# Performance work log

Hardware: AMD Instinct MI355X
Metric: run time of the kernel (lower is better)

## Reference

```python
import jax, jax.numpy as jnp
import numpy as np

PT_SEQ_LEN = 16    # hardcoded hw_seq_len in the module
THETA = 10000.0


def _rope_tables(head_dim):
    # VisionRotaryEmbeddingFast with dim = head_dim // 2, pt_seq_len = ft_seq_len = 16
    d = head_dim // 2                                   # 32
    freqs = 1.0 / (THETA ** (np.arange(0, d, 2, dtype=np.float64) / d))  # (d//2,) = (16,)
    t = np.arange(PT_SEQ_LEN, dtype=np.float64)         # t / ft * pt = arange since ft==pt
    f = np.einsum('i,j->ij', t, freqs)                  # (16, 16)
    f = np.repeat(f, 2, axis=-1)                        # (16, 32)  '... n -> ... (n r)'
    fa = np.broadcast_to(f[:, None, :], (PT_SEQ_LEN, PT_SEQ_LEN, d))
    fb = np.broadcast_to(f[None, :, :], (PT_SEQ_LEN, PT_SEQ_LEN, d))
    full = np.concatenate([fa, fb], axis=-1).reshape(-1, head_dim)  # (256, head_dim)
    return (jnp.asarray(np.cos(full), dtype=jnp.float32),
            jnp.asarray(np.sin(full), dtype=jnp.float32))


def _rotate_half(x):
    # '... (d r) -> ... d r', r=2; (x1, x2) -> (-x2, x1)
    x = x.reshape(*x.shape[:-1], -1, 2)
    x1, x2 = x[..., 0], x[..., 1]
    return jnp.stack((-x2, x1), axis=-1).reshape(*x.shape[:-2], -1)


def _apply_rope(t, cos, sin):
    # t: (B, H, N, hd); cos/sin: (N, hd)
    return t * cos + _rotate_half(t) * sin


def setup_inputs() -> dict:
    key = jax.random.key(0)
    ks = jax.random.split(key, 5)
    B, N, dim, sem = 64, 256, 1024, 768
    return {
        'q': jax.random.normal(ks[0], (B, N, dim), dtype=jnp.float32),
        'kv': jax.random.normal(ks[1], (B, N, sem), dtype=jnp.float32),
        'Wq': jax.random.normal(ks[2], (dim, dim), dtype=jnp.float32) * 0.02,
        'Wkv': jax.random.normal(ks[3], (sem, 2 * dim), dtype=jnp.float32) * 0.02,
        'Wproj': jax.random.normal(ks[4], (dim, dim), dtype=jnp.float32) * 0.02,
        'bproj': jnp.zeros((dim,), dtype=jnp.float32),
    }


def reference(q, kv, Wq, Wkv, Wproj, bproj):
    B, N, C = q.shape
    H = 16
    hd = C // H
    cos, sin = _rope_tables(hd)

    qh = (q @ Wq).reshape(B, N, H, hd).transpose(0, 2, 1, 3)        # (B,H,N,hd)
    kvh = (kv @ Wkv).reshape(B, N, 2, H, hd).transpose(2, 0, 3, 1, 4)
    k, v = kvh[0], kvh[1]                                           # (B,H,N,hd)

    qh = _apply_rope(qh, cos, sin)
    k = _apply_rope(k, cos, sin)

    scale = 1.0 / jnp.sqrt(jnp.float32(hd))  # F.sdpa default scale
    logits = jnp.einsum('bhqd,bhkd->bhqk', qh, k) * scale
    attn = jax.nn.softmax(logits, axis=-1)
    out = jnp.einsum('bhqk,bhkd->bhqd', attn, v)                    # (B,H,N,hd)
    out = out.transpose(0, 2, 1, 3).reshape(B, N, C)
    return out @ Wproj + bproj
```

## Files before the change

### kernel.cpp

```cpp
#include <hip/hip_runtime.h>
#include <hip/hip_bf16.h>
#include <math.h>


typedef unsigned int uint;
typedef __attribute__((ext_vector_type(4)))  short s16x4;
typedef __attribute__((ext_vector_type(8)))  short s16x8;
typedef __attribute__((ext_vector_type(16))) short s16x16;
typedef __attribute__((ext_vector_type(4)))  float f32x4;

#define AS1 __attribute__((address_space(1)))
#define AS3 __attribute__((address_space(3)))

__device__ __forceinline__ short f2bf(float x){
  union{float f;uint u;}v; v.f=x;
  return (short)((v.u + 0x7FFFu + ((v.u>>16)&1u))>>16);
}
__device__ __forceinline__ float bf2f(short s){
  union{float f;uint u;}v; v.u=((uint)(unsigned short)s)<<16; return v.f;
}
__device__ __forceinline__ uint packbf(float a,float b){
  return (uint)(unsigned short)f2bf(a) | ((uint)(unsigned short)f2bf(b)<<16);
}
__device__ __forceinline__ void gl_lds16(const void* g, void* l){
  __builtin_amdgcn_global_load_lds((const AS1 uint*)g, (AS3 uint*)l, 16, 0, 0);
}
__device__ __forceinline__ s16x8 ld16(const short* p){ return *(const s16x8*)p; }

__global__ void k_detect(const uint* q, int* flag){
  __shared__ int cnt;
  if(threadIdx.x==0) cnt=0;
  __syncthreads();
  int c=0;
  for(int i=threadIdx.x;i<4096;i+=256){
    uint e=(q[i]>>7)&0xFFu;
    if(e>=120u && e<=130u) c++;
  }
  atomicAdd(&cnt,c);
  __syncthreads();
  if(threadIdx.x==0) *flag = (cnt>2048)?0:1;
}

__global__ void k_convert(const void* src, short* dst, long n8, const int* flag){
  int f=*flag;
  long stride=(long)gridDim.x*blockDim.x;
  for(long i=(long)blockIdx.x*blockDim.x+threadIdx.x;i<n8;i+=stride){
    s16x8 o;
    if(f){
      const float4* s=(const float4*)src;
      float4 a=s[i*2], b=s[i*2+1];
      o[0]=f2bf(a.x);o[1]=f2bf(a.y);o[2]=f2bf(a.z);o[3]=f2bf(a.w);
      o[4]=f2bf(b.x);o[5]=f2bf(b.y);o[6]=f2bf(b.z);o[7]=f2bf(b.w);
    }else{
      o=((const s16x8*)src)[i];
    }
    ((s16x8*)dst)[i]=o;
  }
}

__global__ void k_transpose(const void* W, short* WT, int K, int Nn, const int* flag){
  int f=*flag;
  long total=(long)Nn*(K/8);
  long stride=(long)gridDim.x*blockDim.x;
  for(long idx=(long)blockIdx.x*blockDim.x+threadIdx.x;idx<total;idx+=stride){
    int n=(int)(idx%Nn); int kc=(int)(idx/Nn); int k0=kc*8;
    s16x8 o;
    #pragma unroll
    for(int j=0;j<8;j++){
      o[j]= f ? f2bf(((const float*)W)[(long)(k0+j)*Nn+n])
              : ((const short*)W)[(long)(k0+j)*Nn+n];
    }
    *(s16x8*)&WT[(long)n*K+k0]=o;
  }
}

__global__ void k_tables(float* cosT, float* sinT){
  int t=blockIdx.x*blockDim.x+threadIdx.x;
  if(t>=256*64) return;
  int n=t>>6, d=t&63;
  int i=n>>4, j=n&15;
  int p=(d&31)>>1;
  double fr=pow(10000.0, -(double)(2*p)/32.0);
  double tt=(d<32)?(double)i:(double)j;
  double a=tt*fr;
  cosT[t]=(float)cos(a);
  sinT[t]=(float)sin(a);
}

__global__ void k_bias(const void* b, float* bo, const int* flag){
  int t=blockIdx.x*blockDim.x+threadIdx.x;
  if(t<1024) bo[t] = (*flag)? ((const float*)b)[t] : bf2f(((const short*)b)[t]);
}

#define BAR   __builtin_amdgcn_s_barrier()
#define LGKM0 asm volatile("s_waitcnt lgkmcnt(0)" ::: "memory")
#define VMC4  asm volatile("s_waitcnt vmcnt(4)" ::: "memory")
#define PRIO1 __builtin_amdgcn_s_setprio(1)
#define PRIO0 __builtin_amdgcn_s_setprio(0)

#define MM(H,V,BR) do{ \
  _Pragma("unroll") for(int ks_=0;ks_<2;ks_++){ \
    _Pragma("unroll") for(int mf_=0;mf_<4;mf_++){ \
      _Pragma("unroll") for(int nf_=0;nf_<2;nf_++){ \
        acc[(H)*4+mf_][(V)*2+nf_]=__builtin_amdgcn_mfma_f32_16x16x32_bf16( \
          aR[mf_][ks_],BR[nf_][ks_],acc[(H)*4+mf_][(V)*2+nf_],0,0,0); \
  }}} }while(0)

#define HALFIT(BUF,TA,TB) do{ \
  const short* RA=&lds[BUF][0][wm][0]; \
  const short* RB=&lds[BUF][1][0][0]; \
  ldA(RA,0,aR); ldB(RB,0,bR0); stage(0,0,TA); \
  BAR; LGKM0; PRIO1; MM(0,0,bR0); PRIO0; BAR; \
  ldB(RB,1,bR1); stage(0,1,TA); \
  BAR; LGKM0; PRIO1; MM(0,1,bR1); PRIO0; BAR; \
  ldA(RA,1,aR); stage(1,0,TB); \
  BAR; LGKM0; PRIO1; MM(1,1,bR1); PRIO0; BAR; \
  stage(1,1,TB); \
  BAR; PRIO1; MM(1,0,bR0); PRIO0; VMC4; BAR; \
}while(0)

template<int EPI>
__launch_bounds__(512,2)
__global__ void k_gemm8(const short* __restrict__ A, const short* __restrict__ BT,
                        const int Kdim, const int lgN,
                        short* __restrict__ out0, short* __restrict__ out1,
                        const float* __restrict__ cosT, const float* __restrict__ sinT,
                        const float* __restrict__ bias, const int* __restrict__ flag,
                        void* __restrict__ dout){
  __shared__ __align__(16) short lds[2][2][2][8192];
  const int tid=threadIdx.x, lane=tid&63, wave=tid>>6;
  const int li=lane&15, gq=lane>>4;
  const int wm=wave>>2, wn=wave&3;
  const int nwg=gridDim.x, cpx=nwg>>3;
  const int wg=((int)blockIdx.x&7)*cpx+((int)blockIdx.x>>3);
  const int tn=wg&((1<<lgN)-1), tm=wg>>lgN;
  const int NT=Kdim>>6;
  const short* Ag=A+(long)tm*256*Kdim;
  const short* Bg=BT+(long)tn*256*Kdim;
  const int fl=(EPI==2)? *flag : 0;
  f32x4 acc[8][4]={};
  s16x8 aR[4][2], bR0[2][2], bR1[2][2];

  auto stage=[&](int op,int hf,int kt){
    int ktw=(kt>=NT)?kt-NT:kt;
    const short* G=(op? Bg:Ag)+((long)(hf*128))*Kdim+ktw*64;
    short* R=&lds[kt&1][op][hf][0];
    #pragma unroll
    for(int l=0;l<2;l++){
      int lr=l*64+wave*8+(lane>>3);
      int c=(lane&7)^((lr>>1)&7);
      gl_lds16(G+(long)lr*Kdim+c*8, R+l*4096+wave*512+lane*8);
    }
  };
  auto ldA=[&](const short* R,int h,s16x8 (&a)[4][2]){
    #pragma unroll
    for(int mf=0;mf<4;mf++){
      int lr=(h*4+mf)*16+li;
      int sw=(lr>>1)&7;
      #pragma unroll
      for(int ks=0;ks<2;ks++){
        int slot=(ks*4+gq)^sw;
        a[mf][ks]=*(const s16x8*)&R[lr*64+slot*8];
      }
    }
  };
  auto ldB=[&](const short* R0,int v,s16x8 (&b)[2][2]){
    #pragma unroll
    for(int nf=0;nf<2;nf++){
      int row=wn*64+(v*2+nf)*16+li;
      const short* R=R0+(row>>7)*8192;
      int lr=row&127;
      int sw=(lr>>1)&7;
      #pragma unroll
      for(int ks=0;ks<2;ks++){
        int slot=(ks*4+gq)^sw;
        b[nf][ks]=*(const s16x8*)&R[lr*64+slot*8];
      }
    }
  };

  stage(1,0,0); stage(1,1,0); stage(0,0,0); stage(0,1,0);
  stage(1,0,1); stage(1,1,1);
  VMC4;
  BAR;

  for(int t=0;t<NT;t+=2){
    HALFIT(0, t+1, t+2);
    HALFIT(1, t+2, t+3);
  }

  const int mb=tm*256+wm*128, nb=tn*256+wn*64;
  #pragma unroll
  for(int mf=0;mf<8;mf++)
  #pragma unroll
  for(int nf=0;nf<4;nf++){
    const int m0=mb+mf*16+gq*4;
    const int n=nb+nf*16+li;
    if(EPI==0){
      #pragma unroll
      for(int r=0;r<4;r++){
        float v=acc[mf][nf][r];
        int m=m0+r, b=m>>8, nn=m&255, h=n>>6, d=n&63;
        float part=__shfl_xor(v,1);
        float c=cosT[(nn<<6)+d], s=sinT[(nn<<6)+d];
        float rot=(d&1)?part:-part;
        out0[(((long)(b*16+h)*256+nn)<<6)+d]=f2bf((v*c+rot*s)*0.125f);
      }
    } else if(EPI==1){
      if(n<1024){
        #pragma unroll
        for(int r=0;r<4;r++){
          float v=acc[mf][nf][r];
          int m=m0+r, b=m>>8, nn=m&255, h=(n>>6)&15, d=n&63;
          float part=__shfl_xor(v,1);
          float c=cosT[(nn<<6)+d], s=sinT[(nn<<6)+d];
          float rot=(d&1)?part:-part;
          out0[(((long)(b*16+h)*256+nn)<<6)+d]=f2bf(v*c+rot*s);
        }
      }else{
        int h=(n>>6)&15, d=n&63, b=m0>>8, nn0=m0&255;
        s16x4 pk;
        #pragma unroll
        for(int r=0;r<4;r++) pk[r]=f2bf(acc[mf][nf][r]);
        *(s16x4*)&out1[(((long)(b*16+h)*64+d)<<8)+nn0]=pk;
      }
    } else {
      #pragma unroll
      for(int r=0;r<4;r++){
        float o=acc[mf][nf][r]+bias[n];
        long idx=((long)(m0+r)<<10)+n;
        if(fl) ((float*)dout)[idx]=o;
        else   ((short*)dout)[idx]=f2bf(o);
      }
    }
  }
}

__launch_bounds__(256,2)
__global__ void k_attn(const short* qh, const short* kb, const short* vt, short* out){
  __shared__ __align__(16) short ol[4][64][72];
  int bh=blockIdx.x, b=bh>>4, h=bh&15;
  int tid=threadIdx.x, lane=tid&63, wave=tid>>6;
  const short* Q=qh+(long)bh*256*64;
  const short* K=kb+(long)bh*256*64;
  const short* VT=vt+(long)bh*64*256;

  s16x8 qf[4][2];
  #pragma unroll
  for(int qb=0;qb<4;qb++)
    #pragma unroll
    for(int kk=0;kk<2;kk++)
      qf[qb][kk]=ld16(Q+(wave*64+qb*16+(lane&15))*64+kk*32+(lane>>4)*8);

  f32x4 o[4][4]={};
  float mrow[4]={-INFINITY,-INFINITY,-INFINITY,-INFINITY};
  float srow[4]={0.f,0.f,0.f,0.f};
  const int g=lane>>4;
  const int srcA=(lane&15)|((((g<<1))&3)<<4);
  const int srcB=(lane&15)|((((g<<1)|1)&3)<<4);
  const bool hi=(g>=2);

  for(int kt=0;kt<8;kt++){
    s16x8 kA[2][2];
    #pragma unroll
    for(int f=0;f<2;f++)
      #pragma unroll
      for(int kk=0;kk<2;kk++)
        kA[f][kk]=ld16(K+(kt*32+f*16+(lane&15))*64+kk*32+(lane>>4)*8);
    f32x4 st[2][4]={};
    #pragma unroll
    for(int kk=0;kk<2;kk++)
      #pragma unroll
      for(int f=0;f<2;f++)
        #pragma unroll
        for(int qb=0;qb<4;qb++)
          st[f][qb]=__builtin_amdgcn_mfma_f32_16x16x32_bf16(kA[f][kk],qf[qb][kk],st[f][qb],0,0,0);

    s16x8 pb[4];
    #pragma unroll
    for(int qb=0;qb<4;qb++){
      float pm=st[0][qb][0];
      #pragma unroll
      for(int f=0;f<2;f++)
        #pragma unroll
        for(int r=0;r<4;r++) pm=fmaxf(pm,st[f][qb][r]);
      pm=fmaxf(pm,__shfl_xor(pm,16));
      pm=fmaxf(pm,__shfl_xor(pm,32));
      float mn=fmaxf(mrow[qb],pm);
      float al=__expf(mrow[qb]-mn);
      mrow[qb]=mn;
      float p00=__expf(st[0][qb][0]-mn), p01=__expf(st[0][qb][1]-mn);
      float p02=__expf(st[0][qb][2]-mn), p03=__expf(st[0][qb][3]-mn);
      float p10=__expf(st[1][qb][0]-mn), p11=__expf(st[1][qb][1]-mn);
      float p12=__expf(st[1][qb][2]-mn), p13=__expf(st[1][qb][3]-mn);
      float ps=p00+p01+p02+p03+p10+p11+p12+p13;
      ps+=__shfl_xor(ps,16);
      ps+=__shfl_xor(ps,32);
      srow[qb]=srow[qb]*al+ps;
      #pragma unroll
      for(int db=0;db<4;db++){
        o[db][qb][0]*=al; o[db][qb][1]*=al; o[db][qb][2]*=al; o[db][qb][3]*=al;
      }
      uint pk00=packbf(p00,p01), pk01=packbf(p02,p03);
      uint pk10=packbf(p10,p11), pk11=packbf(p12,p13);
      uint s00=(uint)__shfl((int)pk00,srcA), s10=(uint)__shfl((int)pk10,srcA);
      uint s01=(uint)__shfl((int)pk01,srcA), s11=(uint)__shfl((int)pk11,srcA);
      uint t00=(uint)__shfl((int)pk00,srcB), t10=(uint)__shfl((int)pk10,srcB);
      uint t01=(uint)__shfl((int)pk01,srcB), t11=(uint)__shfl((int)pk11,srcB);
      union{s16x8 v;uint u[4];}pp;
      pp.u[0]=hi?s10:s00;
      pp.u[1]=hi?s11:s01;
      pp.u[2]=hi?t10:t00;
      pp.u[3]=hi?t11:t01;
      pb[qb]=pp.v;
    }
    s16x8 vA[4];
    #pragma unroll
    for(int db=0;db<4;db++)
      vA[db]=ld16(VT+(db*16+(lane&15))*256+kt*32+(lane>>4)*8);
    #pragma unroll
    for(int db=0;db<4;db++)
      #pragma unroll
      for(int qb=0;qb<4;qb++)
        o[db][qb]=__builtin_amdgcn_mfma_f32_16x16x32_bf16(vA[db],pb[qb],o[db][qb],0,0,0);
  }

  #pragma unroll
  for(int db=0;db<4;db++)
    #pragma unroll
    for(int qb=0;qb<4;qb++)
      #pragma unroll
      for(int r=0;r<4;r++){
        int d=db*16+(lane>>4)*4+r;
        int q=qb*16+(lane&15);
        ol[wave][q][d]=f2bf(o[db][qb][r]/srow[qb]);
      }
  __syncthreads();
  #pragma unroll
  for(int it=0;it<8;it++){
    int q=wave*64+it*8+(lane>>3);
    int cc=lane&7;
    s16x8 x=*(const s16x8*)&ol[wave][it*8+(lane>>3)][cc*8];
    *(s16x8*)&out[((long)(b*256+q)<<10)+h*64+cc*8]=x;
  }
}

extern "C" void kernel_launch(void* const* d_in, const int* in_sizes, int n_in,
                              void* d_out, int out_size, void* d_ws, size_t ws_size,
                              hipStream_t stream){
  const long M=16384;
  char* ws=(char*)d_ws;
  size_t off=0;
  auto alloc=[&](size_t b){ void* p=ws+off; off+=(b+255)&~(size_t)255; return p; };
  int*   flag =(int*)  alloc(256);
  float* cosT =(float*)alloc(256*64*4);
  float* sinT =(float*)alloc(256*64*4);
  float* biasF=(float*)alloc(1024*4);
  short* qbf  =(short*)alloc((size_t)M*1024*2);
  short* kvbf =(short*)alloc((size_t)M*768*2);
  short* WqT  =(short*)alloc((size_t)1024*1024*2);
  short* WkvT =(short*)alloc((size_t)2048*768*2);
  short* WpT  =(short*)alloc((size_t)1024*1024*2);
  short* qhB  =(short*)alloc((size_t)16777216*2);
  short* kbuf =(short*)alloc((size_t)16777216*2);
  short* vtb  =(short*)alloc((size_t)16777216*2);

  k_detect<<<1,256,0,stream>>>((const uint*)d_in[0],flag);
  k_tables<<<64,256,0,stream>>>(cosT,sinT);
  k_bias<<<4,256,0,stream>>>(d_in[5],biasF,flag);
  k_convert<<<2048,256,0,stream>>>(d_in[0],qbf,(long)M*1024/8,flag);
  k_convert<<<2048,256,0,stream>>>(d_in[1],kvbf,(long)M*768/8,flag);
  k_transpose<<<512,256,0,stream>>>(d_in[2],WqT,1024,1024,flag);
  k_transpose<<<768,256,0,stream>>>(d_in[3],WkvT,768,2048,flag);
  k_transpose<<<512,256,0,stream>>>(d_in[4],WpT,1024,1024,flag);

  k_gemm8<0><<<256,512,0,stream>>>(qbf ,WqT ,1024,2,qhB ,nullptr,cosT,sinT,biasF,flag,nullptr);
  k_gemm8<1><<<512,512,0,stream>>>(kvbf,WkvT, 768,3,kbuf,vtb    ,cosT,sinT,biasF,flag,nullptr);
  k_attn<<<1024,256,0,stream>>>(qhB,kbuf,vtb,qbf);
  k_gemm8<2><<<256,512,0,stream>>>(qbf ,WpT ,1024,2,nullptr,nullptr,cosT,sinT,biasF,flag,d_out);
}
```

Before: 270.8 us.

## Merge prep kernels, fuse Q and KV GEMMs, switch to 32x32x16 MFMA

Folds the table, bias, conversion and transpose kernels into one grid-stride prep kernel, which removes several launches. The Q and KV projection GEMMs now run as a single 768-workgroup launch that picks its role per workgroup. The GEMM inner loop moves from 16x16x32 to 32x32x16 bf16 MFMA, with the LDS fragment loads and epilogue index maths rewritten for the new accumulator layout. The larger accumulator tiles could raise register pressure, and the epilogue row mapping has to match the 32x32 output layout exactly for results to stay correct.

```diff
diff --git a/kernel.cpp b/kernel.cpp
--- a/kernel.cpp
+++ b/kernel.cpp
@@ -6,8 +6,8 @@
 typedef unsigned int uint;
 typedef __attribute__((ext_vector_type(4)))  short s16x4;
 typedef __attribute__((ext_vector_type(8)))  short s16x8;
-typedef __attribute__((ext_vector_type(16))) short s16x16;
 typedef __attribute__((ext_vector_type(4)))  float f32x4;
+typedef __attribute__((ext_vector_type(16))) float f32x16;
 
 #define AS1 __attribute__((address_space(1)))
 #define AS3 __attribute__((address_space(3)))
@@ -41,55 +41,55 @@
   if(threadIdx.x==0) *flag = (cnt>2048)?0:1;
 }
 
-__global__ void k_convert(const void* src, short* dst, long n8, const int* flag){
-  int f=*flag;
-  long stride=(long)gridDim.x*blockDim.x;
-  for(long i=(long)blockIdx.x*blockDim.x+threadIdx.x;i<n8;i+=stride){
-    s16x8 o;
-    if(f){
-      const float4* s=(const float4*)src;
-      float4 a=s[i*2], b=s[i*2+1];
-      o[0]=f2bf(a.x);o[1]=f2bf(a.y);o[2]=f2bf(a.z);o[3]=f2bf(a.w);
-      o[4]=f2bf(b.x);o[5]=f2bf(b.y);o[6]=f2bf(b.z);o[7]=f2bf(b.w);
-    }else{
-      o=((const s16x8*)src)[i];
-    }
-    ((s16x8*)dst)[i]=o;
-  }
-}
-
-__global__ void k_transpose(const void* W, short* WT, int K, int Nn, const int* flag){
-  int f=*flag;
-  long total=(long)Nn*(K/8);
-  long stride=(long)gridDim.x*blockDim.x;
-  for(long idx=(long)blockIdx.x*blockDim.x+threadIdx.x;idx<total;idx+=stride){
-    int n=(int)(idx%Nn); int kc=(int)(idx/Nn); int k0=kc*8;
-    s16x8 o;
-    #pragma unroll
-    for(int j=0;j<8;j++){
-      o[j]= f ? f2bf(((const float*)W)[(long)(k0+j)*Nn+n])
-              : ((const short*)W)[(long)(k0+j)*Nn+n];
-    }
-    *(s16x8*)&WT[(long)n*K+k0]=o;
-  }
-}
-
-__global__ void k_tables(float* cosT, float* sinT){
-  int t=blockIdx.x*blockDim.x+threadIdx.x;
-  if(t>=256*64) return;
-  int n=t>>6, d=t&63;
-  int i=n>>4, j=n&15;
-  int p=(d&31)>>1;
-  double fr=pow(10000.0, -(double)(2*p)/32.0);
-  double tt=(d<32)?(double)i:(double)j;
-  double a=tt*fr;
-  cosT[t]=(float)cos(a);
-  sinT[t]=(float)sin(a);
-}
-
-__global__ void k_bias(const void* b, float* bo, const int* flag){
-  int t=blockIdx.x*blockDim.x+threadIdx.x;
-  if(t<1024) bo[t] = (*flag)? ((const float*)b)[t] : bf2f(((const short*)b)[t]);
+__global__ void k_prep(const void* Wq, const void* Wkv, const void* Wp,
+                       const void* bsrc, const void* qsrc, const void* kvsrc,
+                       short* WqT, short* WkvT, short* WpT, float* biasF,
+                       float* cosT, float* sinT, short* qbf, short* kvbf,
+                       const int* flag){
+  const int f=*flag;
+  const long S0=16384, S1=S0+1024, S2=S1+131072, S3=S2+196608, S4=S3+131072,
+             S5=S4+2097152, S6=S5+1572864;
+  const long stride=(long)gridDim.x*blockDim.x;
+  for(long idx=(long)blockIdx.x*blockDim.x+threadIdx.x; idx<S6; idx+=stride){
+    if(idx<S0){
+      int t=(int)idx, n=t>>6, d=t&63;
+      int i=n>>4, j=n&15, p=(d&31)>>1;
+      double fr=pow(10000.0, -(double)(2*p)/32.0);
+      double tt=(d<32)?(double)i:(double)j;
+      double a=tt*fr;
+      cosT[t]=(float)cos(a); sinT[t]=(float)sin(a);
+    } else if(idx<S1){
+      int t=(int)(idx-S0);
+      biasF[t]= f ? ((const float*)bsrc)[t] : bf2f(((const short*)bsrc)[t]);
+    } else if(idx<S4){
+      const void* W; short* WT; int K,Nn; long g;
+      if(idx<S2){ W=Wq;  WT=WqT;  K=1024; Nn=1024; g=idx-S1; }
+      else if(idx<S3){ W=Wkv; WT=WkvT; K=768; Nn=2048; g=idx-S2; }
+      else { W=Wp;  WT=WpT;  K=1024; Nn=1024; g=idx-S3; }
+      int n=(int)(g%Nn); int k0=(int)(g/Nn)*8;
+      s16x8 o;
+      #pragma unroll
+      for(int j=0;j<8;j++){
+        o[j]= f ? f2bf(((const float*)W)[(long)(k0+j)*Nn+n])
+                : ((const short*)W)[(long)(k0+j)*Nn+n];
+      }
+      *(s16x8*)&WT[(long)n*K+k0]=o;
+    } else {
+      const void* src; short* dst; long i;
+      if(idx<S5){ src=qsrc; dst=qbf; i=idx-S4; }
+      else { src=kvsrc; dst=kvbf; i=idx-S5; }
+      s16x8 o;
+      if(f){
+        const float4* s=(const float4*)src;
+        float4 a=s[i*2], b=s[i*2+1];
+        o[0]=f2bf(a.x);o[1]=f2bf(a.y);o[2]=f2bf(a.z);o[3]=f2bf(a.w);
+        o[4]=f2bf(b.x);o[5]=f2bf(b.y);o[6]=f2bf(b.z);o[7]=f2bf(b.w);
+      }else{
+        o=((const s16x8*)src)[i];
+      }
+      ((s16x8*)dst)[i]=o;
+    }
+  }
 }
 
 #define BAR   __builtin_amdgcn_s_barrier()
@@ -99,12 +99,11 @@
 #define PRIO0 __builtin_amdgcn_s_setprio(0)
 
 #define MM(H,V,BR) do{ \
-  _Pragma("unroll") for(int ks_=0;ks_<2;ks_++){ \
-    _Pragma("unroll") for(int mf_=0;mf_<4;mf_++){ \
-      _Pragma("unroll") for(int nf_=0;nf_<2;nf_++){ \
-        acc[(H)*4+mf_][(V)*2+nf_]=__builtin_amdgcn_mfma_f32_16x16x32_bf16( \
-          aR[mf_][ks_],BR[nf_][ks_],acc[(H)*4+mf_][(V)*2+nf_],0,0,0); \
-  }}} }while(0)
+  _Pragma("unroll") for(int ks_=0;ks_<4;ks_++){ \
+    _Pragma("unroll") for(int mf_=0;mf_<2;mf_++){ \
+      acc[(H)*2+mf_][V]=__builtin_amdgcn_mfma_f32_32x32x16_bf16( \
+        aR[mf_][ks_],BR[ks_],acc[(H)*2+mf_][V],0,0,0); \
+  }} }while(0)
 
 #define HALFIT(BUF,TA,TB) do{ \
   const short* RA=&lds[BUF][0][wm][0]; \
@@ -119,27 +118,36 @@
   BAR; PRIO1; MM(1,0,bR0); PRIO0; VMC4; BAR; \
 }while(0)
 
-template<int EPI>
+template<int MODE>
 __launch_bounds__(512,2)
-__global__ void k_gemm8(const short* __restrict__ A, const short* __restrict__ BT,
-                        const int Kdim, const int lgN,
+__global__ void k_gemm8(const short* __restrict__ Aq, const short* __restrict__ Bq,
+                        const short* __restrict__ Akv, const short* __restrict__ Bkv,
                         short* __restrict__ out0, short* __restrict__ out1,
+                        short* __restrict__ out2,
                         const float* __restrict__ cosT, const float* __restrict__ sinT,
                         const float* __restrict__ bias, const int* __restrict__ flag,
                         void* __restrict__ dout){
   __shared__ __align__(16) short lds[2][2][2][8192];
   const int tid=threadIdx.x, lane=tid&63, wave=tid>>6;
-  const int li=lane&15, gq=lane>>4;
+  const int ln31=lane&31, l5=lane>>5;
   const int wm=wave>>2, wn=wave&3;
   const int nwg=gridDim.x, cpx=nwg>>3;
   const int wg=((int)blockIdx.x&7)*cpx+((int)blockIdx.x>>3);
-  const int tn=wg&((1<<lgN)-1), tm=wg>>lgN;
+  int role, tm, tn, Kdim;
+  const short *Ag, *Bg;
+  if(MODE==1){
+    role=2; tn=wg&3; tm=wg>>2; Kdim=1024;
+    Ag=Aq+(long)tm*256*1024; Bg=Bq+(long)tn*256*1024;
+  } else {
+    if(wg<256){ role=0; tn=wg&3; tm=wg>>2; Kdim=1024;
+      Ag=Aq+(long)tm*256*1024; Bg=Bq+(long)tn*256*1024; }
+    else { role=1; int w=wg-256; tn=w&7; tm=w>>3; Kdim=768;
+      Ag=Akv+(long)tm*256*768; Bg=Bkv+(long)tn*256*768; }
+  }
   const int NT=Kdim>>6;
-  const short* Ag=A+(long)tm*256*Kdim;
-  const short* Bg=BT+(long)tn*256*Kdim;
-  const int fl=(EPI==2)? *flag : 0;
-  f32x4 acc[8][4]={};
-  s16x8 aR[4][2], bR0[2][2], bR1[2][2];
+  const int fl=(MODE==1)? *flag : 0;
+  f32x16 acc[4][2]={};
+  s16x8 aR[2][4], bR0[4], bR1[4];
 
   auto stage=[&](int op,int hf,int kt){
     int ktw=(kt>=NT)?kt-NT:kt;
@@ -152,30 +160,27 @@
       gl_lds16(G+(long)lr*Kdim+c*8, R+l*4096+wave*512+lane*8);
     }
   };
-  auto ldA=[&](const short* R,int h,s16x8 (&a)[4][2]){
-    #pragma unroll
-    for(int mf=0;mf<4;mf++){
-      int lr=(h*4+mf)*16+li;
+  auto ldA=[&](const short* R,int h,s16x8 (&a)[2][4]){
+    #pragma unroll
+    for(int mf=0;mf<2;mf++){
+      int lr=h*64+mf*32+ln31;
       int sw=(lr>>1)&7;
       #pragma unroll
-      for(int ks=0;ks<2;ks++){
-        int slot=(ks*4+gq)^sw;
+      for(int ks=0;ks<4;ks++){
+        int slot=(ks*2+l5)^sw;
         a[mf][ks]=*(const s16x8*)&R[lr*64+slot*8];
       }
     }
   };
-  auto ldB=[&](const short* R0,int v,s16x8 (&b)[2][2]){
-    #pragma unroll
-    for(int nf=0;nf<2;nf++){
-      int row=wn*64+(v*2+nf)*16+li;
-      const short* R=R0+(row>>7)*8192;
-      int lr=row&127;
-      int sw=(lr>>1)&7;
-      #pragma unroll
-      for(int ks=0;ks<2;ks++){
-        int slot=(ks*4+gq)^sw;
-        b[nf][ks]=*(const s16x8*)&R[lr*64+slot*8];
-      }
+  auto ldB=[&](const short* R0,int v,s16x8 (&b)[4]){
+    int row=wn*64+v*32+ln31;
+    const short* R=R0+(row>>7)*8192;
+    int lr=row&127;
+    int sw=(lr>>1)&7;
+    #pragma unroll
+    for(int ks=0;ks<4;ks++){
+      int slot=(ks*2+l5)^sw;
+      b[ks]=*(const s16x8*)&R[lr*64+slot*8];
     }
   };
 
@@ -191,46 +196,57 @@
 
   const int mb=tm*256+wm*128, nb=tn*256+wn*64;
   #pragma unroll
-  for(int mf=0;mf<8;mf++)
-  #pragma unroll
-  for(int nf=0;nf<4;nf++){
-    const int m0=mb+mf*16+gq*4;
-    const int n=nb+nf*16+li;
-    if(EPI==0){
-      #pragma unroll
-      for(int r=0;r<4;r++){
+  for(int mf=0;mf<4;mf++)
+  #pragma unroll
+  for(int nf=0;nf<2;nf++){
+    const int n=nb+nf*32+ln31;
+    if(MODE==1){
+      float bi=bias[n];
+      #pragma unroll
+      for(int r=0;r<16;r++){
+        int m=mb+mf*32+(r&3)+8*(r>>2)+4*l5;
+        float o=acc[mf][nf][r]+bi;
+        long idx=((long)m<<10)+n;
+        if(fl) ((float*)dout)[idx]=o;
+        else   ((short*)dout)[idx]=f2bf(o);
+      }
+    } else if(role==0){
+      int h=n>>6, d=n&63;
+      float c=cosT[0], s=0.f;
+      #pragma unroll
+      for(int r=0;r<16;r++){
+        int m=mb+mf*32+(r&3)+8*(r>>2)+4*l5;
+        int b=m>>8, nn=m&255;
         float v=acc[mf][nf][r];
-        int m=m0+r, b=m>>8, nn=m&255, h=n>>6, d=n&63;
         float part=__shfl_xor(v,1);
-        float c=cosT[(nn<<6)+d], s=sinT[(nn<<6)+d];
+        c=cosT[(nn<<6)+d]; s=sinT[(nn<<6)+d];
         float rot=(d&1)?part:-part;
         out0[(((long)(b*16+h)*256+nn)<<6)+d]=f2bf((v*c+rot*s)*0.125f);
       }
-    } else if(EPI==1){
+    } else {
       if(n<1024){
+        int h=(n>>6)&15, d=n&63;
         #pragma unroll
-        for(int r=0;r<4;r++){
+        for(int r=0;r<16;r++){
+          int m=mb+mf*32+(r&3)+8*(r>>2)+4*l5;
+          int b=m>>8, nn=m&255;
           float v=acc[mf][nf][r];
-          int m=m0+r, b=m>>8, nn=m&255, h=(n>>6)&15, d=n&63;
           float part=__shfl_xor(v,1);
           float c=cosT[(nn<<6)+d], s=sinT[(nn<<6)+d];
           float rot=(d&1)?part:-part;
-          out0[(((long)(b*16+h)*256+nn)<<6)+d]=f2bf(v*c+rot*s);
+          out1[(((long)(b*16+h)*256+nn)<<6)+d]=f2bf(v*c+rot*s);
         }
       }else{
-        int h=(n>>6)&15, d=n&63, b=m0>>8, nn0=m0&255;
-        s16x4 pk;
+        int h=(n>>6)&15, d=n&63;
         #pragma unroll
-        for(int r=0;r<4;r++) pk[r]=f2bf(acc[mf][nf][r]);
-        *(s16x4*)&out1[(((long)(b*16+h)*64+d)<<8)+nn0]=pk;
-      }
-    } else {
-      #pragma unroll
-      for(int r=0;r<4;r++){
-        float o=acc[mf][nf][r]+bias[n];
-        long idx=((long)(m0+r)<<10)+n;
-        if(fl) ((float*)dout)[idx]=o;
-        else   ((short*)dout)[idx]=f2bf(o);
+        for(int rq=0;rq<4;rq++){
+          int m0=mb+mf*32+8*rq+4*l5;
+          int b=m0>>8, nn0=m0&255;
+          s16x4 pk;
+          #pragma unroll
+          for(int j=0;j<4;j++) pk[j]=f2bf(acc[mf][nf][rq*4+j]);
+          *(s16x4*)&out2[(((long)(b*16+h)*64+d)<<8)+nn0]=pk;
+        }
       }
     }
   }
@@ -366,16 +382,11 @@
   short* vtb  =(short*)alloc((size_t)16777216*2);
 
   k_detect<<<1,256,0,stream>>>((const uint*)d_in[0],flag);
-  k_tables<<<64,256,0,stream>>>(cosT,sinT);
-  k_bias<<<4,256,0,stream>>>(d_in[5],biasF,flag);
-  k_convert<<<2048,256,0,stream>>>(d_in[0],qbf,(long)M*1024/8,flag);
-  k_convert<<<2048,256,0,stream>>>(d_in[1],kvbf,(long)M*768/8,flag);
-  k_transpose<<<512,256,0,stream>>>(d_in[2],WqT,1024,1024,flag);
-  k_transpose<<<768,256,0,stream>>>(d_in[3],WkvT,768,2048,flag);
-  k_transpose<<<512,256,0,stream>>>(d_in[4],WpT,1024,1024,flag);
-
-  k_gemm8<0><<<256,512,0,stream>>>(qbf ,WqT ,1024,2,qhB ,nullptr,cosT,sinT,biasF,flag,nullptr);
-  k_gemm8<1><<<512,512,0,stream>>>(kvbf,WkvT, 768,3,kbuf,vtb    ,cosT,sinT,biasF,flag,nullptr);
+  k_prep<<<2048,256,0,stream>>>(d_in[2],d_in[3],d_in[4],d_in[5],d_in[0],d_in[1],
+                                WqT,WkvT,WpT,biasF,cosT,sinT,qbf,kvbf,flag);
+  k_gemm8<0><<<768,512,0,stream>>>(qbf,WqT,kvbf,WkvT,qhB,kbuf,vtb,
+                                   cosT,sinT,biasF,flag,nullptr);
   k_attn<<<1024,256,0,stream>>>(qhB,kbuf,vtb,qbf);
-  k_gemm8<2><<<256,512,0,stream>>>(qbf ,WpT ,1024,2,nullptr,nullptr,cosT,sinT,biasF,flag,d_out);
-}
+  k_gemm8<1><<<256,512,0,stream>>>(qbf,WpT,nullptr,nullptr,nullptr,nullptr,nullptr,
+                                   cosT,sinT,biasF,flag,d_out);
+}
```

Result: faster. 263.9 us (-2.6%).
